# Optimization experiments

Hardware: AMD Instinct MI355X
Metric: run time of the kernel (lower is better)

Reference implementation:

```python
import jax, jax.numpy as jnp
import numpy as np

B, IN_BITS, NUM_LUTS, K = 1024, 4096, 16384, 6

def setup_inputs() -> dict:
    key = jax.random.key(0)
    k1, k2, k3 = jax.random.split(key, 3)
    x_bits = jax.random.uniform(k1, (B, IN_BITS), dtype=jnp.float32)
    table = jax.random.normal(k2, (NUM_LUTS, 2 ** K), dtype=jnp.float32) * 0.01
    conn_idx = jax.random.randint(k3, (NUM_LUTS, K), 0, IN_BITS, dtype=jnp.int64)
    return {"x_bits": x_bits, "table": table, "conn_idx": conn_idx}

def reference(x_bits, table, conn_idx):
    # threshold to binary bits: [B, IN_BITS]
    bits01 = (x_bits > 0.5)
    # gather connected bits per LUT: [B, NUM_LUTS, K]
    bits = bits01[:, conn_idx]
    # bit-pack (MSB first, matching idx = idx*2 + bit loop): [B, NUM_LUTS]
    powers = (2 ** jnp.arange(K - 1, -1, -1, dtype=jnp.int32))  # [K]
    idx = jnp.sum(bits.astype(jnp.int32) * powers, axis=-1)
    # per-LUT table lookup: table[l, idx[b, l]]
    lut_ids = jnp.arange(NUM_LUTS, dtype=jnp.int32)[None, :]  # [1, NUM_LUTS]
    out = table[lut_ids, idx]  # [B, NUM_LUTS]
    return jax.nn.sigmoid(out)
```

## Files before the change

### kernel.cpp

```cpp
#include <hip/hip_runtime.h>
#include <hip/hip_bf16.h>

constexpr int B        = 1024;
constexpr int IN_BITS  = 4096;
constexpr int NUM_LUTS = 16384;
constexpr int K        = 6;

constexpr int TPB        = 256;
constexpr int LUTS_PER_B = 256;
constexpr int CHUNKS     = 8;
constexpr int BCH        = B / CHUNKS;

constexpr int PACK_BLOCKS = (IN_BITS / TPB) * (B / 32);
constexpr int TBL_BLOCKS  = NUM_LUTS / 64;

__global__ __launch_bounds__(TPB) void prep_kernel(
    const float* __restrict__ x, const float* __restrict__ table,
    unsigned* __restrict__ packedT, float* __restrict__ tableT)
{
    __shared__ float tile[64][65];
    const int tid = threadIdx.x;
    const int blk = blockIdx.x;

    if (blk < PACK_BLOCKS) {
        const int pos = (blk % (IN_BITS / TPB)) * TPB + tid;
        const int g   = blk / (IN_BITS / TPB);
        const float* xp = x + (size_t)g * 32 * IN_BITS + pos;
        unsigned word = 0;
#pragma unroll
        for (int j = 0; j < 32; ++j)
            word |= (xp[(size_t)j * IN_BITS] > 0.5f) ? (1u << j) : 0u;
        packedT[(size_t)g * IN_BITS + pos] = word;
    } else {
        const int bt = blk - PACK_BLOCKS;
        const int l0 = bt * 64;
        const float4* src = (const float4*)(table + (size_t)l0 * 64);
#pragma unroll
        for (int i = 0; i < 4; ++i) {
            int q = tid + i * 256;
            float4 v = src[q];
            int l = q >> 4;
            int e = (q & 15) * 4;
            tile[l][e + 0] = v.x; tile[l][e + 1] = v.y;
            tile[l][e + 2] = v.z; tile[l][e + 3] = v.w;
        }
        __syncthreads();
#pragma unroll
        for (int i = 0; i < 4; ++i) {
            int q  = tid + i * 256;
            int e  = q >> 4;
            int lc = (q & 15) * 4;
            float4 v;
            v.x = 1.0f / (1.0f + __expf(-tile[lc + 0][e]));
            v.y = 1.0f / (1.0f + __expf(-tile[lc + 1][e]));
            v.z = 1.0f / (1.0f + __expf(-tile[lc + 2][e]));
            v.w = 1.0f / (1.0f + __expf(-tile[lc + 3][e]));
            ((float4*)(tableT + (size_t)e * NUM_LUTS + l0))[q & 15] = v;
        }
    }
}

__global__ __launch_bounds__(TPB, 2) void lut_kernel(
    const int*      __restrict__ conn,
    const unsigned* __restrict__ packedT,
    const float*    __restrict__ tableT,
    float*          __restrict__ out)
{
    __shared__ float tbl[64 * LUTS_PER_B];

    const int tid = threadIdx.x;
    const int l0  = blockIdx.x * LUTS_PER_B;
    const int l   = l0 + tid;

    {
        float4* dst = (float4*)tbl;
#pragma unroll
        for (int i = 0; i < 16; ++i) {
            int q = tid + i * 256;
            int e = q >> 6;
            int c = q & 63;
            dst[q] = ((const float4*)(tableT + (size_t)e * NUM_LUTS + l0))[c];
        }
    }

    int c[K];
#pragma unroll
    for (int k = 0; k < K; ++k) c[k] = conn[(size_t)l * K + k];

    __syncthreads();

    const int bbase = blockIdx.y * BCH;
    float* op = out + (size_t)bbase * NUM_LUTS + l;

    for (int g = 0; g < BCH / 32; ++g) {
        const unsigned* pr = packedT + (size_t)(bbase / 32 + g) * IN_BITS;
        unsigned w[K];
#pragma unroll
        for (int k = 0; k < K; ++k) w[k] = pr[c[k]];

#pragma unroll
        for (int j = 0; j < 32; ++j) {
            int idx = 0;
#pragma unroll
            for (int k = 0; k < K; ++k)
                idx = (idx << 1) | (int)((w[k] >> j) & 1u);
            float v = tbl[idx * LUTS_PER_B + tid];
            __builtin_nontemporal_store(v, op);
            op += NUM_LUTS;
        }
    }
}

extern "C" void kernel_launch(void* const* d_in, const int* in_sizes, int n_in,
                              void* d_out, int out_size, void* d_ws, size_t ws_size,
                              hipStream_t stream)
{
    const float* x_bits = (const float*)d_in[0];
    const float* table  = (const float*)d_in[1];
    const int*   conn   = (const int*)d_in[2];
    float* out = (float*)d_out;

    unsigned* packedT = (unsigned*)d_ws;
    float*    tableT  = (float*)((char*)d_ws + 512 * 1024);

    prep_kernel<<<PACK_BLOCKS + TBL_BLOCKS, TPB, 0, stream>>>(
        x_bits, table, packedT, tableT);

    dim3 g2(NUM_LUTS / LUTS_PER_B, CHUNKS);
    lut_kernel<<<g2, TPB, 0, stream>>>(conn, packedT, tableT, out);
}
```

Baseline: 94.88 us.

## Store sigmoid table as bf16 to halve LDS footprint and raise occupancy

The precomputed sigmoid table is now stored in bf16 in both the workspace and LDS, which halves the per-block shared memory from 64KB to 32KB. That allows 4 blocks per CU instead of 2. The batch is split into 16 chunks to put more blocks in the grid, and the group loop is unrolled. The output keeps only bf16 precision (about 3 significant digits), which may exceed tolerance on sigmoid outputs near 0.5.

```diff
diff --git a/kernel.cpp b/kernel.cpp
--- a/kernel.cpp
+++ b/kernel.cpp
@@ -8,15 +8,20 @@
 
 constexpr int TPB        = 256;
 constexpr int LUTS_PER_B = 256;
-constexpr int CHUNKS     = 8;
+constexpr int CHUNKS     = 16;
 constexpr int BCH        = B / CHUNKS;
 
 constexpr int PACK_BLOCKS = (IN_BITS / TPB) * (B / 32);
 constexpr int TBL_BLOCKS  = NUM_LUTS / 64;
 
+__device__ inline unsigned short f2bf(float f) {
+    unsigned u = __float_as_uint(f);
+    return (unsigned short)((u + 0x7FFFu + ((u >> 16) & 1u)) >> 16);
+}
+
 __global__ __launch_bounds__(TPB) void prep_kernel(
     const float* __restrict__ x, const float* __restrict__ table,
-    unsigned* __restrict__ packedT, float* __restrict__ tableT)
+    unsigned* __restrict__ packedT, unsigned short* __restrict__ tableT)
 {
     __shared__ float tile[64][65];
     const int tid = threadIdx.x;
@@ -50,36 +55,36 @@
             int q  = tid + i * 256;
             int e  = q >> 4;
             int lc = (q & 15) * 4;
-            float4 v;
-            v.x = 1.0f / (1.0f + __expf(-tile[lc + 0][e]));
-            v.y = 1.0f / (1.0f + __expf(-tile[lc + 1][e]));
-            v.z = 1.0f / (1.0f + __expf(-tile[lc + 2][e]));
-            v.w = 1.0f / (1.0f + __expf(-tile[lc + 3][e]));
-            ((float4*)(tableT + (size_t)e * NUM_LUTS + l0))[q & 15] = v;
+            ushort4 v;
+            v.x = f2bf(1.0f / (1.0f + __expf(-tile[lc + 0][e])));
+            v.y = f2bf(1.0f / (1.0f + __expf(-tile[lc + 1][e])));
+            v.z = f2bf(1.0f / (1.0f + __expf(-tile[lc + 2][e])));
+            v.w = f2bf(1.0f / (1.0f + __expf(-tile[lc + 3][e])));
+            ((ushort4*)(tableT + (size_t)e * NUM_LUTS + l0))[q & 15] = v;
         }
     }
 }
 
-__global__ __launch_bounds__(TPB, 2) void lut_kernel(
-    const int*      __restrict__ conn,
-    const unsigned* __restrict__ packedT,
-    const float*    __restrict__ tableT,
-    float*          __restrict__ out)
+__global__ __launch_bounds__(TPB, 4) void lut_kernel(
+    const int*            __restrict__ conn,
+    const unsigned*       __restrict__ packedT,
+    const unsigned short* __restrict__ tableT,
+    float*                __restrict__ out)
 {
-    __shared__ float tbl[64 * LUTS_PER_B];
+    __shared__ unsigned short tbl[64 * LUTS_PER_B];
 
     const int tid = threadIdx.x;
     const int l0  = blockIdx.x * LUTS_PER_B;
     const int l   = l0 + tid;
 
     {
-        float4* dst = (float4*)tbl;
+        uint4* dst = (uint4*)tbl;
 #pragma unroll
-        for (int i = 0; i < 16; ++i) {
+        for (int i = 0; i < 8; ++i) {
             int q = tid + i * 256;
-            int e = q >> 6;
-            int c = q & 63;
-            dst[q] = ((const float4*)(tableT + (size_t)e * NUM_LUTS + l0))[c];
+            int e = q >> 5;
+            int p = q & 31;
+            dst[q] = ((const uint4*)(tableT + (size_t)e * NUM_LUTS + l0))[p];
         }
     }
 
@@ -92,6 +97,7 @@
     const int bbase = blockIdx.y * BCH;
     float* op = out + (size_t)bbase * NUM_LUTS + l;
 
+#pragma unroll
     for (int g = 0; g < BCH / 32; ++g) {
         const unsigned* pr = packedT + (size_t)(bbase / 32 + g) * IN_BITS;
         unsigned w[K];
@@ -104,7 +110,8 @@
 #pragma unroll
             for (int k = 0; k < K; ++k)
                 idx = (idx << 1) | (int)((w[k] >> j) & 1u);
-            float v = tbl[idx * LUTS_PER_B + tid];
+            unsigned short h = tbl[idx * LUTS_PER_B + tid];
+            float v = __uint_as_float((unsigned)h << 16);
             __builtin_nontemporal_store(v, op);
             op += NUM_LUTS;
         }
@@ -120,8 +127,8 @@
     const int*   conn   = (const int*)d_in[2];
     float* out = (float*)d_out;
 
-    unsigned* packedT = (unsigned*)d_ws;
-    float*    tableT  = (float*)((char*)d_ws + 512 * 1024);
+    unsigned*       packedT = (unsigned*)d_ws;
+    unsigned short* tableT  = (unsigned short*)((char*)d_ws + 512 * 1024);
 
     prep_kernel<<<PACK_BLOCKS + TBL_BLOCKS, TPB, 0, stream>>>(
         x_bits, table, packedT, tableT);
```

Result: no change. 93.55 us (-1.4%).
